# Optimization experiments

Hardware: AMD Instinct MI355X
Metric: run time of the kernel (lower is better)

Reference implementation:

```python
import jax, jax.numpy as jnp
import numpy as np

B, N, C, H, TR = 2, 5000, 256, 8, 2
M = N // TR  # reduced KV length from Conv1d(data_len, data_len//tr, 1)
DK = C // H


def setup_inputs() -> dict:
    key = jax.random.key(0)
    ks = jax.random.split(key, 10)
    s = 0.02
    return {
        "x": jax.random.normal(ks[0], (B, N, C), jnp.float32),
        "Wq": jax.random.normal(ks[1], (C, C), jnp.float32) * s,
        "bq": jnp.zeros((C,), jnp.float32),
        "Wk": jax.random.normal(ks[2], (C, C), jnp.float32) * s,
        "bk": jnp.zeros((C,), jnp.float32),
        "Wv": jax.random.normal(ks[3], (C, C), jnp.float32) * s,
        "bv": jnp.zeros((C,), jnp.float32),
        "Wc": jax.random.normal(ks[4], (M, N), jnp.float32) * (1.0 / np.sqrt(N)),
        "bc": jnp.zeros((M,), jnp.float32),
        "gamma": jnp.ones((C,), jnp.float32),
        "beta": jnp.zeros((C,), jnp.float32),
    }


def _layernorm(x, gamma, beta, eps=1e-5):
    mu = jnp.mean(x, axis=-1, keepdims=True)
    var = jnp.mean(jnp.square(x - mu), axis=-1, keepdims=True)
    return gamma * (x - mu) * jax.lax.rsqrt(var + eps) + beta


def reference(x, Wq, bq, Wk, bk, Wv, bv, Wc, bc, gamma, beta):
    b, n, c = x.shape
    # Q projection: (B, H, N, DK)
    q = (x @ Wq.T + bq).reshape(b, n, H, DK).transpose(0, 2, 1, 3)
    # Spatial reduction: Conv1d with kernel size 1 over the N (channel) dim,
    # then LayerNorm over feature dim C
    x_ = jnp.einsum('mn,bnc->bmc', Wc, x) + bc[None, :, None]
    x_ = _layernorm(x_, gamma, beta)
    k = (x_ @ Wk.T + bk).reshape(b, -1, H, DK).transpose(0, 2, 1, 3)  # (B,H,M,DK)
    v = (x_ @ Wv.T + bv).reshape(b, -1, H, DK).transpose(0, 2, 1, 3)  # (B,H,M,DK)
    # Naive attention (full score matrix, as in the original module)
    scores = jnp.einsum('bhnd,bhmd->bhnm', q, k) / jnp.sqrt(jnp.asarray(DK, x.dtype))
    p = jax.nn.softmax(scores, axis=-1)
    out = jnp.einsum('bhnm,bhmd->bhnd', p, v)
    # note: output_linear is declared in __init__ but never applied in forward
    return out.transpose(0, 2, 1, 3).reshape(b, n, c)
```

## Files before the change

kernel.cpp:

```cpp
#include <hip/hip_runtime.h>
#include <hip/hip_bf16.h>
#include <hip/hip_fp16.h>
#include <math.h>

constexpr int B = 2;
constexpr int N = 5000;
constexpr int C = 256;
constexpr int H = 8;
constexpr int DK = 32;
constexpr int M = 2500;
constexpr int MP = 2512;
constexpr int KSTEPS = 157;
constexpr int SPLIT = 8;
constexpr int MTILES = 79;
constexpr float QSCALE = 0.2550598692503365f;

typedef __attribute__((ext_vector_type(8))) short bf16x8;
typedef __attribute__((ext_vector_type(4))) float f32x4;

static __device__ __forceinline__ ushort f2bf(float f) {
  __hip_bfloat16 h = __float2bfloat16(f);
  return *reinterpret_cast<ushort*>(&h);
}

static __device__ __forceinline__ float fastexp2(float x) {
#if __has_builtin(__builtin_amdgcn_exp2f)
  return __builtin_amdgcn_exp2f(x);
#else
  return exp2f(x);
#endif
}

__global__ __launch_bounds__(256) void wcast(const float* __restrict__ Wq,
                                             const float* __restrict__ Wk,
                                             const float* __restrict__ Wv,
                                             ushort* __restrict__ W16) {
  const float* src = (blockIdx.y == 0) ? Wq : (blockIdx.y == 1) ? Wk : Wv;
  const int idx = blockIdx.x * 1024 + threadIdx.x * 4;
  const float4 v = *reinterpret_cast<const float4*>(src + idx);
  ushort4 o;
  o.x = f2bf(v.x); o.y = f2bf(v.y); o.z = f2bf(v.z); o.w = f2bf(v.w);
  *reinterpret_cast<ushort4*>(W16 + (size_t)blockIdx.y * C * C + idx) = o;
}

__global__ __launch_bounds__(256) void xt_cast(const float* __restrict__ x,
                                               ushort* __restrict__ xTt,
                                               ushort* __restrict__ xb16) {
  const int n0 = blockIdx.x * 64, c0 = blockIdx.y * 64, b = blockIdx.z;
  const int tid = threadIdx.x;
  __shared__ ushort T[64][68];
  const float* xb = x + (size_t)b * N * C;
#pragma unroll
  for (int i = 0; i < 4; ++i) {
    const int nl = (tid >> 4) + i * 16;
    const int cg = (tid & 15) * 4;
    float4 v = {0.f, 0.f, 0.f, 0.f};
    const bool ok = (n0 + nl) < N;
    if (ok) v = *reinterpret_cast<const float4*>(xb + (size_t)(n0 + nl) * C + c0 + cg);
    ushort4 u;
    u.x = f2bf(v.x); u.y = f2bf(v.y); u.z = f2bf(v.z); u.w = f2bf(v.w);
    T[nl][cg + 0] = u.x; T[nl][cg + 1] = u.y; T[nl][cg + 2] = u.z; T[nl][cg + 3] = u.w;
    if (ok)
      *reinterpret_cast<ushort4*>(xb16 + ((size_t)b * N + n0 + nl) * C + c0 + cg) = u;
  }
  __syncthreads();
  ushort* ob = xTt + (size_t)b * KSTEPS * C * 32;
  const int cl = tid & 63, ng = tid >> 6;
#pragma unroll
  for (int j = 0; j < 2; ++j) {
    const int nstart = ng * 16 + j * 8;
    const int n = n0 + nstart;
    if (n >= KSTEPS * 32) continue;
    const int ks = n >> 5, kk = n & 31;
    ushort vals[8];
#pragma unroll
    for (int jj = 0; jj < 8; ++jj) vals[jj] = T[nstart + jj][cl];
    *reinterpret_cast<bf16x8*>(ob + ((size_t)ks * C + (c0 + cl)) * 32 + kk) =
        *reinterpret_cast<const bf16x8*>(vals);
  }
}

__global__ __launch_bounds__(256) void conv_mfma(const float* __restrict__ Wc,
                                                 const ushort* __restrict__ xTt,
                                                 ushort* __restrict__ xpart) {
  const int s = blockIdx.x & 7;
  const int mt = blockIdx.x >> 3;
  const int m0 = mt * 32;
  const int tid = threadIdx.x, w = tid >> 6, l = tid & 63;
  const int lr = l & 15, lg = l >> 4;
  f32x4 acc[16];
#pragma unroll
  for (int i = 0; i < 16; ++i) acc[i] = (f32x4){0.f, 0.f, 0.f, 0.f};
  const int row0 = m0 + lr, row1 = m0 + 16 + lr;
  const bool ok0 = row0 < M, ok1 = row1 < M;
  const float* ap0 = Wc + (size_t)(ok0 ? row0 : 0) * N + lg * 8;
  const float* ap1 = Wc + (size_t)(ok1 ? row1 : 0) * N + lg * 8;
  const int crow = w * 64 + lr;

#pragma unroll 2
  for (int ks = s; ks < KSTEPS; ks += SPLIT) {
    const int n0 = ks * 32;
    const bool kok = (n0 + lg * 8) < N;
    bf16x8 a0 = {0, 0, 0, 0, 0, 0, 0, 0}, a1 = {0, 0, 0, 0, 0, 0, 0, 0};
    if (ok0 && kok) {
      const float4 v0 = *reinterpret_cast<const float4*>(ap0 + n0);
      const float4 v1 = *reinterpret_cast<const float4*>(ap0 + n0 + 4);
      ushort u[8];
      u[0] = f2bf(v0.x); u[1] = f2bf(v0.y); u[2] = f2bf(v0.z); u[3] = f2bf(v0.w);
      u[4] = f2bf(v1.x); u[5] = f2bf(v1.y); u[6] = f2bf(v1.z); u[7] = f2bf(v1.w);
      a0 = *reinterpret_cast<const bf16x8*>(u);
    }
    if (ok1 && kok) {
      const float4 v0 = *reinterpret_cast<const float4*>(ap1 + n0);
      const float4 v1 = *reinterpret_cast<const float4*>(ap1 + n0 + 4);
      ushort u[8];
      u[0] = f2bf(v0.x); u[1] = f2bf(v0.y); u[2] = f2bf(v0.z); u[3] = f2bf(v0.w);
      u[4] = f2bf(v1.x); u[5] = f2bf(v1.y); u[6] = f2bf(v1.z); u[7] = f2bf(v1.w);
      a1 = *reinterpret_cast<const bf16x8*>(u);
    }
    bf16x8 bf[8];
#pragma unroll
    for (int ct = 0; ct < 4; ++ct)
#pragma unroll
      for (int bb = 0; bb < 2; ++bb)
        bf[ct * 2 + bb] = *reinterpret_cast<const bf16x8*>(
            xTt + (((size_t)bb * KSTEPS + ks) * C + crow + ct * 16) * 32 + lg * 8);
#pragma unroll
    for (int ct = 0; ct < 4; ++ct)
#pragma unroll
      for (int bb = 0; bb < 2; ++bb) {
        acc[(0 * 4 + ct) * 2 + bb] =
            __builtin_amdgcn_mfma_f32_16x16x32_bf16(a0, bf[ct * 2 + bb], acc[(0 * 4 + ct) * 2 + bb], 0, 0, 0);
        acc[(1 * 4 + ct) * 2 + bb] =
            __builtin_amdgcn_mfma_f32_16x16x32_bf16(a1, bf[ct * 2 + bb], acc[(1 * 4 + ct) * 2 + bb], 0, 0, 0);
      }
  }

#pragma unroll
  for (int mf = 0; mf < 2; ++mf)
#pragma unroll
    for (int ct = 0; ct < 4; ++ct)
#pragma unroll
      for (int bb = 0; bb < 2; ++bb)
#pragma unroll
        for (int i = 0; i < 4; ++i) {
          const int m = m0 + mf * 16 + lg * 4 + i;
          if (m < M) {
            const __half hv = __float2half(acc[(mf * 4 + ct) * 2 + bb][i]);
            xpart[(((size_t)s * B + bb) * M + m) * C + w * 64 + ct * 16 + lr] =
                *reinterpret_cast<const ushort*>(&hv);
          }
        }
}

__global__ __launch_bounds__(256) void ln_kernel(const ushort* __restrict__ xp,
                                                 const float* __restrict__ bc,
                                                 const float* __restrict__ gamma,
                                                 const float* __restrict__ beta,
                                                 ushort* __restrict__ xr16) {
  const int row = blockIdx.x;
  const int tid = threadIdx.x;
  const int b = row / M, m = row - b * M;
  const size_t base = (size_t)row * C;
  float v = bc[m];
#pragma unroll
  for (int s = 0; s < SPLIT; ++s) {
    const ushort us = xp[(((size_t)s * B + b) * M + m) * C + tid];
    v += __half2float(*reinterpret_cast<const __half*>(&us));
  }
  __shared__ float red[8];
  float sum = v;
#pragma unroll
  for (int o = 32; o >= 1; o >>= 1) sum += __shfl_xor(sum, o);
  if ((tid & 63) == 0) red[tid >> 6] = sum;
  __syncthreads();
  const float mu = (red[0] + red[1] + red[2] + red[3]) * (1.f / C);
  const float d = v - mu;
  float s2 = d * d;
#pragma unroll
  for (int o = 32; o >= 1; o >>= 1) s2 += __shfl_xor(s2, o);
  if ((tid & 63) == 0) red[4 + (tid >> 6)] = s2;
  __syncthreads();
  const float var = (red[4] + red[5] + red[6] + red[7]) * (1.f / C);
  xr16[base + tid] = f2bf(gamma[tid] * d * rsqrtf(var + 1e-5f) + beta[tid]);
}

__global__ __launch_bounds__(256) void proj_all(const ushort* __restrict__ xb16,
                                                const ushort* __restrict__ xr16,
                                                const ushort* __restrict__ W16,
                                                const float* __restrict__ bq,
                                                const float* __restrict__ bk,
                                                const float* __restrict__ bv,
                                                ushort* __restrict__ qb,
                                                ushort* __restrict__ kb,
                                                ushort* __restrict__ vt) {
  const int z = blockIdx.z;
  const int R = (z == 0) ? N : M;
  const int totalRows = B * R;
  if (blockIdx.x * 64 >= totalRows) return;
  const ushort* xin = (z == 0) ? xb16 : xr16;
  const ushort* W = W16 + (size_t)z * C * C;
  const float* bias = (z == 0) ? bq : (z == 1) ? bk : bv;
  const int tid = threadIdx.x, w = tid >> 6, l = tid & 63;
  const int lr = l & 15, lg = l >> 4;
  const int r0 = blockIdx.x * 64 + w * 16;
  const int c0 = blockIdx.y * 64;
  const int arow = r0 + lr;
  const bool aok = arow < totalRows;
  f32x4 acc[4] = {{0.f,0.f,0.f,0.f},{0.f,0.f,0.f,0.f},{0.f,0.f,0.f,0.f},{0.f,0.f,0.f,0.f}};
#pragma unroll
  for (int ks = 0; ks < 8; ++ks) {
    bf16x8 af = {0, 0, 0, 0, 0, 0, 0, 0};
    if (aok) af = *reinterpret_cast<const bf16x8*>(xin + (size_t)arow * C + ks * 32 + lg * 8);
#pragma unroll
    for (int ct = 0; ct < 4; ++ct) {
      const bf16x8 bf =
          *reinterpret_cast<const bf16x8*>(W + (size_t)(c0 + ct * 16 + lr) * C + ks * 32 + lg * 8);
      acc[ct] = __builtin_amdgcn_mfma_f32_16x16x32_bf16(af, bf, acc[ct], 0, 0, 0);
    }
  }
#pragma unroll
  for (int ct = 0; ct < 4; ++ct) {
    const int c = c0 + ct * 16 + lr;
    const int h = c >> 5, d = c & 31;
    const float bi = bias[c];
#pragma unroll
    for (int i = 0; i < 4; ++i) {
      const int row = r0 + lg * 4 + i;
      if (row >= totalRows) continue;
      const int bb = (row >= R) ? 1 : 0;
      const int rr = row - bb * R;
      float val = acc[ct][i] + bi;
      if (z == 0) {
        val *= QSCALE;
        qb[(((size_t)bb * H + h) * N + rr) * DK + d] = f2bf(val);
      } else if (z == 1) {
        kb[(((size_t)bb * H + h) * M + rr) * DK + d] = f2bf(val);
      } else {
        vt[(((size_t)bb * H + h) * DK + d) * MP + rr] = f2bf(val);
      }
    }
  }
}

__global__ __launch_bounds__(256) void attn8(const ushort* __restrict__ q,
                                             const ushort* __restrict__ kk,
                                             const ushort* __restrict__ vt,
                                             float* __restrict__ out) {
  const int qt = blockIdx.x, h = blockIdx.y, b = blockIdx.z;
  const int tid = threadIdx.x, w = tid >> 6, l = tid & 63;
  const int lr = l & 15, lg = l >> 4;
  const int n0 = qt * 128 + w * 32;
  __shared__ ushort Plds[4][2][16][74];
  const ushort* qp = q + (size_t)(b * H + h) * N * DK;
  const ushort* kp = kk + (size_t)(b * H + h) * M * DK;
  const ushort* vp = vt + (size_t)(b * H + h) * DK * MP;

  bf16x8 qf0 = {0, 0, 0, 0, 0, 0, 0, 0}, qf1 = {0, 0, 0, 0, 0, 0, 0, 0};
  if (n0 + lr < N) qf0 = *reinterpret_cast<const bf16x8*>(qp + (size_t)(n0 + lr) * DK + lg * 8);
  if (n0 + 16 + lr < N)
    qf1 = *reinterpret_cast<const bf16x8*>(qp + (size_t)(n0 + 16 + lr) * DK + lg * 8);

  f32x4 O0[2] = {{0.f, 0.f, 0.f, 0.f}, {0.f, 0.f, 0.f, 0.f}};
  f32x4 O1[2] = {{0.f, 0.f, 0.f, 0.f}, {0.f, 0.f, 0.f, 0.f}};
  float ps0 = 0.f, ps1 = 0.f;

  constexpr int NT = (M + 63) / 64;
#pragma unroll 1
  for (int t = 0; t < NT; ++t) {
    const int m0 = t * 64;
    const bool full = (m0 + 64) <= M;
    bf16x8 kf[4];
#pragma unroll
    for (int ct = 0; ct < 4; ++ct) {
      const int mr = m0 + ct * 16 + lr;
      if (full || mr < M)
        kf[ct] = *reinterpret_cast<const bf16x8*>(kp + (size_t)mr * DK + lg * 8);
      else
        kf[ct] = (bf16x8){0, 0, 0, 0, 0, 0, 0, 0};
    }
    bf16x8 vf[4];
#pragma unroll
    for (int dt = 0; dt < 2; ++dt) {
      const ushort* vb = vp + (size_t)(dt * 16 + lr) * MP + m0 + lg * 8;
      vf[dt * 2 + 0] = *reinterpret_cast<const bf16x8*>(vb);
      vf[dt * 2 + 1] = *reinterpret_cast<const bf16x8*>(vb + 32);
    }
#pragma unroll
    for (int ct = 0; ct < 4; ++ct) {
      const f32x4 s0 =
          __builtin_amdgcn_mfma_f32_16x16x32_bf16(kf[ct], qf0, (f32x4){0.f, 0.f, 0.f, 0.f}, 0, 0, 0);
      const f32x4 s1 =
          __builtin_amdgcn_mfma_f32_16x16x32_bf16(kf[ct], qf1, (f32x4){0.f, 0.f, 0.f, 0.f}, 0, 0, 0);
      float p0[4], p1[4];
#pragma unroll
      for (int i = 0; i < 4; ++i) {
        const bool mok = full || (m0 + ct * 16 + lg * 4 + i) < M;
        p0[i] = mok ? fastexp2(s0[i]) : 0.f;
        p1[i] = mok ? fastexp2(s1[i]) : 0.f;
        ps0 += p0[i];
        ps1 += p1[i];
      }
      __hip_bfloat162 a01 = __float22bfloat162_rn(make_float2(p0[0], p0[1]));
      __hip_bfloat162 a23 = __float22bfloat162_rn(make_float2(p0[2], p0[3]));
      uint2 u0;
      u0.x = *reinterpret_cast<unsigned*>(&a01);
      u0.y = *reinterpret_cast<unsigned*>(&a23);
      *reinterpret_cast<uint2*>(&Plds[w][0][lr][ct * 16 + lg * 4]) = u0;
      __hip_bfloat162 b01 = __float22bfloat162_rn(make_float2(p1[0], p1[1]));
      __hip_bfloat162 b23 = __float22bfloat162_rn(make_float2(p1[2], p1[3]));
      uint2 u1;
      u1.x = *reinterpret_cast<unsigned*>(&b01);
      u1.y = *reinterpret_cast<unsigned*>(&b23);
      *reinterpret_cast<uint2*>(&Plds[w][1][lr][ct * 16 + lg * 4]) = u1;
    }
    const bf16x8 pa00 = *reinterpret_cast<const bf16x8*>(&Plds[w][0][lr][lg * 8]);
    const bf16x8 pa01 = *reinterpret_cast<const bf16x8*>(&Plds[w][0][lr][32 + lg * 8]);
    const bf16x8 pa10 = *reinterpret_cast<const bf16x8*>(&Plds[w][1][lr][lg * 8]);
    const bf16x8 pa11 = *reinterpret_cast<const bf16x8*>(&Plds[w][1][lr][32 + lg * 8]);
#pragma unroll
    for (int dt = 0; dt < 2; ++dt) {
      O0[dt] = __builtin_amdgcn_mfma_f32_16x16x32_bf16(pa00, vf[dt * 2 + 0], O0[dt], 0, 0, 0);
      O0[dt] = __builtin_amdgcn_mfma_f32_16x16x32_bf16(pa01, vf[dt * 2 + 1], O0[dt], 0, 0, 0);
      O1[dt] = __builtin_amdgcn_mfma_f32_16x16x32_bf16(pa10, vf[dt * 2 + 0], O1[dt], 0, 0, 0);
      O1[dt] = __builtin_amdgcn_mfma_f32_16x16x32_bf16(pa11, vf[dt * 2 + 1], O1[dt], 0, 0, 0);
    }
  }

  ps0 += __shfl_xor(ps0, 16);
  ps0 += __shfl_xor(ps0, 32);
  ps1 += __shfl_xor(ps1, 16);
  ps1 += __shfl_xor(ps1, 32);
  const float inv0 = 1.f / ps0, inv1 = 1.f / ps1;
#pragma unroll
  for (int i = 0; i < 4; ++i) {
    const float iv0 = __shfl(inv0, lg * 4 + i);
    const float iv1 = __shfl(inv1, lg * 4 + i);
    const int r0q = n0 + lg * 4 + i;
    const int r1q = n0 + 16 + lg * 4 + i;
    if (r0q < N) {
      float* ob = out + ((size_t)b * N + r0q) * C + h * DK + lr;
      ob[0] = O0[0][i] * iv0;
      ob[16] = O0[1][i] * iv0;
    }
    if (r1q < N) {
      float* ob = out + ((size_t)b * N + r1q) * C + h * DK + lr;
      ob[0] = O1[0][i] * iv1;
      ob[16] = O1[1][i] * iv1;
    }
  }
}

extern "C" void kernel_launch(void* const* d_in, const int* in_sizes, int n_in,
                              void* d_out, int out_size, void* d_ws, size_t ws_size,
                              hipStream_t stream) {
  (void)in_sizes; (void)n_in; (void)out_size; (void)ws_size;
  const float* x     = (const float*)d_in[0];
  const float* Wq    = (const float*)d_in[1];
  const float* bq    = (const float*)d_in[2];
  const float* Wk    = (const float*)d_in[3];
  const float* bk    = (const float*)d_in[4];
  const float* Wv    = (const float*)d_in[5];
  const float* bv    = (const float*)d_in[6];
  const float* Wc    = (const float*)d_in[7];
  const float* bc    = (const float*)d_in[8];
  const float* gamma = (const float*)d_in[9];
  const float* beta  = (const float*)d_in[10];
  float* out = (float*)d_out;

  char* wsb = (char*)d_ws;
  ushort* xpart = (ushort*)wsb;
  ushort* qb = (ushort*)wsb;
  ushort* kb = (ushort*)(wsb + 5120000);
  ushort* vt = (ushort*)(wsb + 7680000);
  char* p = wsb + 20480000;
  ushort* xTt  = (ushort*)p;
  ushort* xr16 = (ushort*)p;
  p += 5144576;
  ushort* xb16 = (ushort*)p; p += 5120000;
  ushort* W16  = (ushort*)p;

  wcast<<<dim3(64, 3), 256, 0, stream>>>(Wq, Wk, Wv, W16);
  xt_cast<<<dim3((N + 63) / 64, C / 64, B), 256, 0, stream>>>(x, xTt, xb16);
  conv_mfma<<<dim3(MTILES * SPLIT), 256, 0, stream>>>(Wc, xTt, xpart);
  ln_kernel<<<dim3(B * M), 256, 0, stream>>>(xpart, bc, gamma, beta, xr16);
  (void)hipMemsetAsync(vt, 0, (size_t)B * H * DK * MP * 2 + 4096, stream);
  proj_all<<<dim3((B * N + 63) / 64, C / 64, 3), 256, 0, stream>>>(xb16, xr16, W16, bq, bk, bv,
                                                                   qb, kb, vt);
  attn8<<<dim3((N + 127) / 128, H, B), 256, 0, stream>>>(qb, kb, vt, out);
}
```

Measured before the change: 176.1 us.

## Split attention KV range into two halves and combine partial results

The attention kernel now handles half of the KV tiles per block, doubling the grid so the 640-block launch spreads more evenly across CUs. Each half writes unnormalized partial outputs and row sums to workspace. A new combine kernel adds the two partials and divides by the summed denominators. This costs extra global traffic for the partial outputs and one more launch. The LDS row padding also shrinks from 74 to 72, which may change bank conflicts.

```diff
diff --git a/kernel.cpp b/kernel.cpp
--- a/kernel.cpp
+++ b/kernel.cpp
@@ -243,18 +243,24 @@
   }
 }
 
-__global__ __launch_bounds__(256) void attn8(const ushort* __restrict__ q,
+__global__ __launch_bounds__(256) void attn9(const ushort* __restrict__ q,
                                              const ushort* __restrict__ kk,
                                              const ushort* __restrict__ vt,
-                                             float* __restrict__ out) {
-  const int qt = blockIdx.x, h = blockIdx.y, b = blockIdx.z;
+                                             float* __restrict__ o0,
+                                             float* __restrict__ o1,
+                                             float* __restrict__ ps0,
+                                             float* __restrict__ ps1) {
+  const int qt = blockIdx.x, h = blockIdx.y, z = blockIdx.z;
+  const int b = z >> 1, half = z & 1;
   const int tid = threadIdx.x, w = tid >> 6, l = tid & 63;
   const int lr = l & 15, lg = l >> 4;
   const int n0 = qt * 128 + w * 32;
-  __shared__ ushort Plds[4][2][16][74];
+  __shared__ ushort Plds[4][2][16][72];
   const ushort* qp = q + (size_t)(b * H + h) * N * DK;
   const ushort* kp = kk + (size_t)(b * H + h) * M * DK;
   const ushort* vp = vt + (size_t)(b * H + h) * DK * MP;
+  float* op = half ? o1 : o0;
+  float* ps = half ? ps1 : ps0;
 
   bf16x8 qf0 = {0, 0, 0, 0, 0, 0, 0, 0}, qf1 = {0, 0, 0, 0, 0, 0, 0, 0};
   if (n0 + lr < N) qf0 = *reinterpret_cast<const bf16x8*>(qp + (size_t)(n0 + lr) * DK + lg * 8);
@@ -263,11 +269,12 @@
 
   f32x4 O0[2] = {{0.f, 0.f, 0.f, 0.f}, {0.f, 0.f, 0.f, 0.f}};
   f32x4 O1[2] = {{0.f, 0.f, 0.f, 0.f}, {0.f, 0.f, 0.f, 0.f}};
-  float ps0 = 0.f, ps1 = 0.f;
-
-  constexpr int NT = (M + 63) / 64;
+  float ps0r = 0.f, ps1r = 0.f;
+
+  const int tbeg = half ? 20 : 0;
+  const int tend = half ? 40 : 20;
 #pragma unroll 1
-  for (int t = 0; t < NT; ++t) {
+  for (int t = tbeg; t < tend; ++t) {
     const int m0 = t * 64;
     const bool full = (m0 + 64) <= M;
     bf16x8 kf[4];
@@ -298,8 +305,8 @@
         const bool mok = full || (m0 + ct * 16 + lg * 4 + i) < M;
         p0[i] = mok ? fastexp2(s0[i]) : 0.f;
         p1[i] = mok ? fastexp2(s1[i]) : 0.f;
-        ps0 += p0[i];
-        ps1 += p1[i];
+        ps0r += p0[i];
+        ps1r += p1[i];
       }
       __hip_bfloat162 a01 = __float22bfloat162_rn(make_float2(p0[0], p0[1]));
       __hip_bfloat162 a23 = __float22bfloat162_rn(make_float2(p0[2], p0[3]));
@@ -327,28 +334,43 @@
     }
   }
 
-  ps0 += __shfl_xor(ps0, 16);
-  ps0 += __shfl_xor(ps0, 32);
-  ps1 += __shfl_xor(ps1, 16);
-  ps1 += __shfl_xor(ps1, 32);
-  const float inv0 = 1.f / ps0, inv1 = 1.f / ps1;
+  ps0r += __shfl_xor(ps0r, 16);
+  ps0r += __shfl_xor(ps0r, 32);
+  ps1r += __shfl_xor(ps1r, 16);
+  ps1r += __shfl_xor(ps1r, 32);
+  if (lg == 0) {
+    const size_t pbase = ((size_t)b * H + h) * N;
+    if (n0 + lr < N) ps[pbase + n0 + lr] = ps0r;
+    if (n0 + 16 + lr < N) ps[pbase + n0 + 16 + lr] = ps1r;
+  }
 #pragma unroll
   for (int i = 0; i < 4; ++i) {
-    const float iv0 = __shfl(inv0, lg * 4 + i);
-    const float iv1 = __shfl(inv1, lg * 4 + i);
     const int r0q = n0 + lg * 4 + i;
     const int r1q = n0 + 16 + lg * 4 + i;
     if (r0q < N) {
-      float* ob = out + ((size_t)b * N + r0q) * C + h * DK + lr;
-      ob[0] = O0[0][i] * iv0;
-      ob[16] = O0[1][i] * iv0;
+      float* ob = op + ((size_t)b * N + r0q) * C + h * DK + lr;
+      ob[0] = O0[0][i];
+      ob[16] = O0[1][i];
     }
     if (r1q < N) {
-      float* ob = out + ((size_t)b * N + r1q) * C + h * DK + lr;
-      ob[0] = O1[0][i] * iv1;
-      ob[16] = O1[1][i] * iv1;
-    }
-  }
+      float* ob = op + ((size_t)b * N + r1q) * C + h * DK + lr;
+      ob[0] = O1[0][i];
+      ob[16] = O1[1][i];
+    }
+  }
+}
+
+__global__ __launch_bounds__(256) void attn_combine(float* __restrict__ out,
+                                                    const float* __restrict__ o1,
+                                                    const float* __restrict__ ps0,
+                                                    const float* __restrict__ ps1) {
+  const int row = blockIdx.x;
+  const int c = threadIdx.x;
+  const int b = row / N, n = row - b * N;
+  const size_t pidx = ((size_t)b * H + (c >> 5)) * N + n;
+  const float denom = ps0[pidx] + ps1[pidx];
+  const size_t idx = (size_t)row * C + c;
+  out[idx] = (out[idx] + o1[idx]) / denom;
 }
 
 extern "C" void kernel_launch(void* const* d_in, const int* in_sizes, int n_in,
@@ -373,9 +395,12 @@
   ushort* qb = (ushort*)wsb;
   ushort* kb = (ushort*)(wsb + 5120000);
   ushort* vt = (ushort*)(wsb + 7680000);
+  float* ps0 = (float*)(wsb + 10400000);
+  float* ps1 = (float*)(wsb + 10720000);
   char* p = wsb + 20480000;
   ushort* xTt  = (ushort*)p;
   ushort* xr16 = (ushort*)p;
+  float* o1 = (float*)p;
   p += 5144576;
   ushort* xb16 = (ushort*)p; p += 5120000;
   ushort* W16  = (ushort*)p;
@@ -387,5 +412,6 @@
   (void)hipMemsetAsync(vt, 0, (size_t)B * H * DK * MP * 2 + 4096, stream);
   proj_all<<<dim3((B * N + 63) / 64, C / 64, 3), 256, 0, stream>>>(xb16, xr16, W16, bq, bk, bv,
                                                                    qb, kb, vt);
-  attn8<<<dim3((N + 127) / 128, H, B), 256, 0, stream>>>(qb, kb, vt, out);
-}
+  attn9<<<dim3((N + 127) / 128, H, B * 2), 256, 0, stream>>>(qb, kb, vt, out, o1, ps0, ps1);
+  attn_combine<<<dim3(B * N), 256, 0, stream>>>(out, o1, ps0, ps1);
+}
```

After: 177.6 us. Within noise of the previous version (+0.9%).
